# Optimization experiments

Measured on AMD Instinct MI355X. Metric: run time of the kernel, lower is better.

Reference implementation:

```python
import jax, jax.numpy as jnp
from jax import lax
import numpy as np

D = 20            # bits per code -> codebook size K = 2**D
K = 2 ** D
TEMP = 0.005
EPS = 1e-10
XSPLIT = 16
ALPHA = 1.0


def setup_inputs() -> dict:
    key = jax.random.key(0)
    x = jax.random.normal(key, (2, 128, D), dtype=jnp.float32)  # [B, N, d]
    return {"x": x}


def _book_t():
    # Deterministic {-1,+1} codebook, transposed: [D, K]
    idx = jnp.arange(K, dtype=jnp.int32)
    shifts = jnp.arange(D - 1, -1, -1, dtype=jnp.int32)
    bits = ((idx[:, None] >> shifts[None, :]) & 1).astype(jnp.float32)  # [K, D]
    return (bits * 2.0 - 1.0).T  # [D, K]


def _forward(x):
    B, N, _ = x.shape
    book_t = _book_t()                      # [D, K]
    num_splits = N // XSPLIT
    # [num_splits, B, XSPLIT, D] chunks, scanned to bound peak memory (mirrors torch chunking)
    xc = x.reshape(B, num_splits, XSPLIT, D).transpose(1, 0, 2, 3)

    def step(carry, x_chunk):
        entro_mean, mean_probs = carry
        l = (x_chunk @ book_t) / TEMP                    # [B, XSPLIT, K]
        probs = jax.nn.softmax(l, axis=-1)
        log_probs = jax.nn.log_softmax(l + EPS, axis=-1)  # eps shift, as in torch
        entropy = -jnp.sum(probs * log_probs, axis=-1)    # [B, XSPLIT]
        entro_mean = entro_mean + jnp.sum(entropy, axis=-1) / N
        # torch: probs.mean over all but last dim -> [K], broadcast-added to [B,K]
        mean_probs = mean_probs + probs.mean(axis=(0, 1))
        return (entro_mean, mean_probs), None

    init = (jnp.zeros((B,), x.dtype), jnp.zeros((K,), x.dtype))
    (entro_mean, mean_probs), _ = lax.scan(jax.checkpoint(step), init, xc)

    mean_probs = mean_probs / num_splits
    # torch mean_probs rows are identical across batch, so mean over batch == single row value
    mean_entro = -jnp.sum(mean_probs * jnp.log(mean_probs + EPS))
    entro_mean_s = entro_mean.mean()
    entro_loss = ALPHA * entro_mean_s - ALPHA * mean_entro

    q_hard = jnp.where(x > 0, 1.0, -1.0).astype(x.dtype)
    q = x + lax.stop_gradient(q_hard - x)                 # straight-through estimator
    commit_loss = jnp.mean((x - lax.stop_gradient(q)) ** 2)
    return q, entro_mean_s, mean_entro, entro_loss, commit_loss


def reference(x):
    return _forward(x)
```

## Files before the change

kernel.cpp:

```cpp
#include <hip/hip_runtime.h>
#include <math.h>


#define RS 264
#define VTS 260
#define POISON 0xAAAAAAAAu

typedef float f32x4 __attribute__((ext_vector_type(4)));
typedef short bf16x8 __attribute__((ext_vector_type(8)));

__device__ inline unsigned pk_bf16x2(float a, float b) {
  unsigned ua = __float_as_uint(a); ua += 0x7FFFu + ((ua >> 16) & 1u);
  unsigned ub = __float_as_uint(b); ub += 0x7FFFu + ((ub >> 16) & 1u);
  return (ua >> 16) | (ub & 0xFFFF0000u);
}

__global__ __launch_bounds__(256) void lfq_one(
    const float* __restrict__ x, float* __restrict__ out,
    double* __restrict__ entPart, double* __restrict__ comPart,
    double* __restrict__ mePart, unsigned* __restrict__ counter) {
  const int blk = blockIdx.x;
  const int tid = threadIdx.x;

  __shared__ float sP1[20][256];
  __shared__ float sVAH[8][VTS], sVAL[8][VTS];
  __shared__ float sVBH[8][VTS], sVBL[8][VTS];
  __shared__ unsigned short sA[64 * RS];
  __shared__ unsigned short sB[64 * RS];
  __shared__ double red[256];
  __shared__ float hb[20], cb[20];
  __shared__ int lastBlk;

  {
    const int t = tid;
    float xv[20];
    const float4* xp = (const float4*)(x + t * 20);
#pragma unroll
    for (int k = 0; k < 5; ++k) {
      float4 v = xp[k];
      xv[4 * k + 0] = v.x; xv[4 * k + 1] = v.y;
      xv[4 * k + 2] = v.z; xv[4 * k + 3] = v.w;
    }
#pragma unroll
    for (int j = 0; j < 20; ++j) {
      float z = 400.f * xv[j];
      float az = fabsf(z);
      float e = __expf(-az);
      float s = e / (1.f + e);
      sP1[j][t] = (z >= 0.f) ? (1.f - s) : s;
    }
  }
  if (tid < 20) {
    float xv = x[blk * 20 + tid];
    float z = 400.f * xv, az = fabsf(z);
    float e = __expf(-az), s = e / (1.f + e);
    hb[tid] = log1pf(e) + az * s;
    float qv = (xv > 0.f) ? 1.f : -1.f;
    out[blk * 20 + tid] = qv;
    float dx = xv - qv;
    cb[tid] = dx * dx;
  }
  __syncthreads();
  if (tid == 0) {
    float hs = 0.f, cs = 0.f;
#pragma unroll
    for (int j = 0; j < 20; ++j) { hs += hb[j]; cs += cb[j]; }
    entPart[blk] = (double)hs;
    comPart[blk] = (double)cs;
  }

  {
    const int t = tid;
    const int ahi = blk & 15, bhi = blk >> 4;
    float c = 1.f;
#pragma unroll
    for (int j = 0; j < 4; ++j) {
      float p = sP1[j][t];
      c *= ((ahi >> (3 - j)) & 1) ? p : (1.f - p);
    }
#pragma unroll
    for (int j = 0; j < 4; ++j) {
      float p = sP1[10 + j][t];
      c *= ((bhi >> (3 - j)) & 1) ? p : (1.f - p);
    }
    float p4 = sP1[4][t], p5 = sP1[5][t], p6 = sP1[6][t];
    float p7 = sP1[7][t], p8 = sP1[8][t], p9 = sP1[9][t];
    float pe = sP1[14][t], pf = sP1[15][t], pg = sP1[16][t];
    float ph = sP1[17][t], pi = sP1[18][t], pj = sP1[19][t];
#pragma unroll
    for (int g = 0; g < 8; ++g) {
      sVAH[g][t] = c * ((g & 4) ? p4 : 1.f - p4) * ((g & 2) ? p5 : 1.f - p5)
                     * ((g & 1) ? p6 : 1.f - p6);
      sVAL[g][t] =     ((g & 4) ? p7 : 1.f - p7) * ((g & 2) ? p8 : 1.f - p8)
                     * ((g & 1) ? p9 : 1.f - p9);
      sVBH[g][t] =     ((g & 4) ? pe : 1.f - pe) * ((g & 2) ? pf : 1.f - pf)
                     * ((g & 1) ? pg : 1.f - pg);
      sVBL[g][t] =     ((g & 4) ? ph : 1.f - ph) * ((g & 2) ? pi : 1.f - pi)
                     * ((g & 1) ? pj : 1.f - pj);
    }
  }
  __syncthreads();

  {
    const int r = tid & 63, tc = tid >> 6;
    const int gH = r >> 3, gL = r & 7;
    unsigned short* arow = sA + r * RS;
    unsigned short* brow = sB + r * RS;
#pragma unroll
    for (int it = 0; it < 16; ++it) {
      int t = tc * 64 + it * 4;
      float4 h = *(const float4*)&sVAH[gH][t];
      float4 l = *(const float4*)&sVAL[gL][t];
      unsigned lo = pk_bf16x2(h.x * l.x, h.y * l.y);
      unsigned hi = pk_bf16x2(h.z * l.z, h.w * l.w);
      *(uint2*)(arow + t) = make_uint2(lo, hi);
      float4 h2 = *(const float4*)&sVBH[gH][t];
      float4 l2 = *(const float4*)&sVBL[gL][t];
      unsigned lo2 = pk_bf16x2(h2.x * l2.x, h2.y * l2.y);
      unsigned hi2 = pk_bf16x2(h2.z * l2.z, h2.w * l2.w);
      *(uint2*)(brow + t) = make_uint2(lo2, hi2);
    }
  }
  __syncthreads();

  const int lane = tid & 63, w = tid >> 6;
  const int m16 = lane & 15, q = lane >> 4;
  f32x4 acc[4];
#pragma unroll
  for (int ct = 0; ct < 4; ++ct) acc[ct] = (f32x4){0.f, 0.f, 0.f, 0.f};
  const unsigned short* ap = sA + (w * 16 + m16) * RS + q * 8;
  const unsigned short* bp = sB + m16 * RS + q * 8;
#pragma unroll
  for (int ks = 0; ks < 8; ++ks) {
    bf16x8 af = *(const bf16x8*)(ap + ks * 32);
    bf16x8 b0 = *(const bf16x8*)(bp + ks * 32);
    bf16x8 b1 = *(const bf16x8*)(bp + 16 * RS + ks * 32);
    bf16x8 b2 = *(const bf16x8*)(bp + 32 * RS + ks * 32);
    bf16x8 b3 = *(const bf16x8*)(bp + 48 * RS + ks * 32);
    acc[0] = __builtin_amdgcn_mfma_f32_16x16x32_bf16(af, b0, acc[0], 0, 0, 0);
    acc[1] = __builtin_amdgcn_mfma_f32_16x16x32_bf16(af, b1, acc[1], 0, 0, 0);
    acc[2] = __builtin_amdgcn_mfma_f32_16x16x32_bf16(af, b2, acc[2], 0, 0, 0);
    acc[3] = __builtin_amdgcn_mfma_f32_16x16x32_bf16(af, b3, acc[3], 0, 0, 0);
  }

  float ts = 0.f;
#pragma unroll
  for (int ct = 0; ct < 4; ++ct)
#pragma unroll
    for (int i = 0; i < 4; ++i) {
      float m = acc[ct][i] * (1.f / 256.f);
      ts -= m * __logf(m + 1e-10f);
    }
  red[tid] = (double)ts;
  __syncthreads();
  for (int s = 128; s > 0; s >>= 1) {
    if (tid < s) red[tid] += red[tid + s];
    __syncthreads();
  }
  if (tid == 0) {
    mePart[blk] = red[0];
    __threadfence();
    unsigned old = atomicAdd(counter, 1u);
    lastBlk = ((old - POISON) == 255u) ? 1 : 0;
  }
  __syncthreads();

  if (lastBlk) {
    __threadfence();
    __shared__ double r1[256], r2[256], r3[256];
    r1[tid] = entPart[tid];
    r2[tid] = comPart[tid];
    r3[tid] = mePart[tid];
    __syncthreads();
    for (int s = 128; s > 0; s >>= 1) {
      if (tid < s) {
        r1[tid] += r1[tid + s];
        r2[tid] += r2[tid + s];
        r3[tid] += r3[tid + s];
      }
      __syncthreads();
    }
    if (tid == 0) {
      double em = r1[0] / 256.0;
      double cm = r2[0] / 5120.0;
      double me = r3[0];
      out[5120] = (float)em;
      out[5121] = (float)me;
      out[5122] = (float)(em - me);
      out[5123] = (float)cm;
    }
  }
}

extern "C" void kernel_launch(void* const* d_in, const int* in_sizes, int n_in,
                              void* d_out, int out_size, void* d_ws, size_t ws_size,
                              hipStream_t stream) {
  const float* x = (const float*)d_in[0];
  float* out = (float*)d_out;
  char* ws = (char*)d_ws;
  double* entPart = (double*)(ws);
  double* comPart = (double*)(ws + 2048);
  double* mePart  = (double*)(ws + 4096);
  unsigned* counter = (unsigned*)(ws + 6144);

  lfq_one<<<256, 256, 0, stream>>>(x, out, entPart, comPart, mePart, counter);
}
```

Measured before the change: 64.57 us.

## Double block threads and build bf16 panels directly from registers

Each block now runs 512 threads. Half of them build the A-side panel and half the B-side panel, computing the sigmoid probabilities and their products in registers and writing bf16 straight to one shared panel. This removes the intermediate sP1/sVAH/sVAL shared arrays and two barriers. The 64x64 MFMA product is split over 8 waves, each producing two 16x16 tiles, so per-wave latency drops. The costs are a deeper block reduction and scalar 2-byte shared stores that may cause bank conflicts.

```diff
diff --git a/kernel.cpp b/kernel.cpp
--- a/kernel.cpp
+++ b/kernel.cpp
@@ -3,53 +3,29 @@
 
 
 #define RS 264
-#define VTS 260
 #define POISON 0xAAAAAAAAu
 
 typedef float f32x4 __attribute__((ext_vector_type(4)));
 typedef short bf16x8 __attribute__((ext_vector_type(8)));
 
-__device__ inline unsigned pk_bf16x2(float a, float b) {
-  unsigned ua = __float_as_uint(a); ua += 0x7FFFu + ((ua >> 16) & 1u);
-  unsigned ub = __float_as_uint(b); ub += 0x7FFFu + ((ub >> 16) & 1u);
-  return (ua >> 16) | (ub & 0xFFFF0000u);
+__device__ inline unsigned short pk_bf16(float a) {
+  unsigned ua = __float_as_uint(a);
+  ua += 0x7FFFu + ((ua >> 16) & 1u);
+  return (unsigned short)(ua >> 16);
 }
 
-__global__ __launch_bounds__(256) void lfq_one(
+__global__ __launch_bounds__(512) void lfq_one(
     const float* __restrict__ x, float* __restrict__ out,
     double* __restrict__ entPart, double* __restrict__ comPart,
     double* __restrict__ mePart, unsigned* __restrict__ counter) {
   const int blk = blockIdx.x;
   const int tid = threadIdx.x;
 
-  __shared__ float sP1[20][256];
-  __shared__ float sVAH[8][VTS], sVAL[8][VTS];
-  __shared__ float sVBH[8][VTS], sVBL[8][VTS];
-  __shared__ unsigned short sA[64 * RS];
-  __shared__ unsigned short sB[64 * RS];
-  __shared__ double red[256];
+  __shared__ unsigned short sP[128 * RS];
+  __shared__ double red[512];
   __shared__ float hb[20], cb[20];
   __shared__ int lastBlk;
 
-  {
-    const int t = tid;
-    float xv[20];
-    const float4* xp = (const float4*)(x + t * 20);
-#pragma unroll
-    for (int k = 0; k < 5; ++k) {
-      float4 v = xp[k];
-      xv[4 * k + 0] = v.x; xv[4 * k + 1] = v.y;
-      xv[4 * k + 2] = v.z; xv[4 * k + 3] = v.w;
-    }
-#pragma unroll
-    for (int j = 0; j < 20; ++j) {
-      float z = 400.f * xv[j];
-      float az = fabsf(z);
-      float e = __expf(-az);
-      float s = e / (1.f + e);
-      sP1[j][t] = (z >= 0.f) ? (1.f - s) : s;
-    }
-  }
   if (tid < 20) {
     float xv = x[blk * 20 + tid];
     float z = 400.f * xv, az = fabsf(z);
@@ -60,7 +36,46 @@
     float dx = xv - qv;
     cb[tid] = dx * dx;
   }
+
+  {
+    const int side = tid >> 8;
+    const int t = tid & 255;
+    const int jo = side * 10;
+    const int hi4 = side ? (blk >> 4) : (blk & 15);
+
+    float p[10];
+    const float2* xp = (const float2*)(x + t * 20 + jo);
+#pragma unroll
+    for (int k = 0; k < 5; ++k) {
+      float2 v = xp[k];
+      float zz0 = 400.f * v.x, zz1 = 400.f * v.y;
+      float a0 = fabsf(zz0), a1 = fabsf(zz1);
+      float e0 = __expf(-a0), e1 = __expf(-a1);
+      float s0 = e0 / (1.f + e0), s1 = e1 / (1.f + e1);
+      p[2 * k]     = (zz0 >= 0.f) ? (1.f - s0) : s0;
+      p[2 * k + 1] = (zz1 >= 0.f) ? (1.f - s1) : s1;
+    }
+    float c = 1.f;
+#pragma unroll
+    for (int j = 0; j < 4; ++j)
+      c *= ((hi4 >> (3 - j)) & 1) ? p[j] : (1.f - p[j]);
+    float cvh[8], vl[8];
+#pragma unroll
+    for (int g = 0; g < 8; ++g) {
+      cvh[g] = c * ((g & 4) ? p[4] : 1.f - p[4])
+                 * ((g & 2) ? p[5] : 1.f - p[5])
+                 * ((g & 1) ? p[6] : 1.f - p[6]);
+      vl[g]  =     ((g & 4) ? p[7] : 1.f - p[7])
+                 * ((g & 2) ? p[8] : 1.f - p[8])
+                 * ((g & 1) ? p[9] : 1.f - p[9]);
+    }
+    unsigned short* panel = sP + side * 64 * RS;
+#pragma unroll
+    for (int r = 0; r < 64; ++r)
+      panel[r * RS + t] = pk_bf16(cvh[r >> 3] * vl[r & 7]);
+  }
   __syncthreads();
+
   if (tid == 0) {
     float hs = 0.f, cs = 0.f;
 #pragma unroll
@@ -69,91 +84,31 @@
     comPart[blk] = (double)cs;
   }
 
-  {
-    const int t = tid;
-    const int ahi = blk & 15, bhi = blk >> 4;
-    float c = 1.f;
-#pragma unroll
-    for (int j = 0; j < 4; ++j) {
-      float p = sP1[j][t];
-      c *= ((ahi >> (3 - j)) & 1) ? p : (1.f - p);
-    }
-#pragma unroll
-    for (int j = 0; j < 4; ++j) {
-      float p = sP1[10 + j][t];
-      c *= ((bhi >> (3 - j)) & 1) ? p : (1.f - p);
-    }
-    float p4 = sP1[4][t], p5 = sP1[5][t], p6 = sP1[6][t];
-    float p7 = sP1[7][t], p8 = sP1[8][t], p9 = sP1[9][t];
-    float pe = sP1[14][t], pf = sP1[15][t], pg = sP1[16][t];
-    float ph = sP1[17][t], pi = sP1[18][t], pj = sP1[19][t];
-#pragma unroll
-    for (int g = 0; g < 8; ++g) {
-      sVAH[g][t] = c * ((g & 4) ? p4 : 1.f - p4) * ((g & 2) ? p5 : 1.f - p5)
-                     * ((g & 1) ? p6 : 1.f - p6);
-      sVAL[g][t] =     ((g & 4) ? p7 : 1.f - p7) * ((g & 2) ? p8 : 1.f - p8)
-                     * ((g & 1) ? p9 : 1.f - p9);
-      sVBH[g][t] =     ((g & 4) ? pe : 1.f - pe) * ((g & 2) ? pf : 1.f - pf)
-                     * ((g & 1) ? pg : 1.f - pg);
-      sVBL[g][t] =     ((g & 4) ? ph : 1.f - ph) * ((g & 2) ? pi : 1.f - pi)
-                     * ((g & 1) ? pj : 1.f - pj);
-    }
-  }
-  __syncthreads();
-
-  {
-    const int r = tid & 63, tc = tid >> 6;
-    const int gH = r >> 3, gL = r & 7;
-    unsigned short* arow = sA + r * RS;
-    unsigned short* brow = sB + r * RS;
-#pragma unroll
-    for (int it = 0; it < 16; ++it) {
-      int t = tc * 64 + it * 4;
-      float4 h = *(const float4*)&sVAH[gH][t];
-      float4 l = *(const float4*)&sVAL[gL][t];
-      unsigned lo = pk_bf16x2(h.x * l.x, h.y * l.y);
-      unsigned hi = pk_bf16x2(h.z * l.z, h.w * l.w);
-      *(uint2*)(arow + t) = make_uint2(lo, hi);
-      float4 h2 = *(const float4*)&sVBH[gH][t];
-      float4 l2 = *(const float4*)&sVBL[gL][t];
-      unsigned lo2 = pk_bf16x2(h2.x * l2.x, h2.y * l2.y);
-      unsigned hi2 = pk_bf16x2(h2.z * l2.z, h2.w * l2.w);
-      *(uint2*)(brow + t) = make_uint2(lo2, hi2);
-    }
-  }
-  __syncthreads();
-
   const int lane = tid & 63, w = tid >> 6;
   const int m16 = lane & 15, q = lane >> 4;
-  f32x4 acc[4];
-#pragma unroll
-  for (int ct = 0; ct < 4; ++ct) acc[ct] = (f32x4){0.f, 0.f, 0.f, 0.f};
-  const unsigned short* ap = sA + (w * 16 + m16) * RS + q * 8;
-  const unsigned short* bp = sB + m16 * RS + q * 8;
+  const unsigned short* ap = sP + ((w & 3) * 16 + m16) * RS + q * 8;
+  const unsigned short* bp = sP + (64 + (w >> 2) * 32 + m16) * RS + q * 8;
+  f32x4 acc0 = {0.f, 0.f, 0.f, 0.f}, acc1 = {0.f, 0.f, 0.f, 0.f};
 #pragma unroll
   for (int ks = 0; ks < 8; ++ks) {
     bf16x8 af = *(const bf16x8*)(ap + ks * 32);
     bf16x8 b0 = *(const bf16x8*)(bp + ks * 32);
     bf16x8 b1 = *(const bf16x8*)(bp + 16 * RS + ks * 32);
-    bf16x8 b2 = *(const bf16x8*)(bp + 32 * RS + ks * 32);
-    bf16x8 b3 = *(const bf16x8*)(bp + 48 * RS + ks * 32);
-    acc[0] = __builtin_amdgcn_mfma_f32_16x16x32_bf16(af, b0, acc[0], 0, 0, 0);
-    acc[1] = __builtin_amdgcn_mfma_f32_16x16x32_bf16(af, b1, acc[1], 0, 0, 0);
-    acc[2] = __builtin_amdgcn_mfma_f32_16x16x32_bf16(af, b2, acc[2], 0, 0, 0);
-    acc[3] = __builtin_amdgcn_mfma_f32_16x16x32_bf16(af, b3, acc[3], 0, 0, 0);
+    acc0 = __builtin_amdgcn_mfma_f32_16x16x32_bf16(af, b0, acc0, 0, 0, 0);
+    acc1 = __builtin_amdgcn_mfma_f32_16x16x32_bf16(af, b1, acc1, 0, 0, 0);
   }
 
   float ts = 0.f;
 #pragma unroll
-  for (int ct = 0; ct < 4; ++ct)
-#pragma unroll
-    for (int i = 0; i < 4; ++i) {
-      float m = acc[ct][i] * (1.f / 256.f);
-      ts -= m * __logf(m + 1e-10f);
-    }
+  for (int i = 0; i < 4; ++i) {
+    float m0 = acc0[i] * (1.f / 256.f);
+    ts -= m0 * __logf(m0 + 1e-10f);
+    float m1 = acc1[i] * (1.f / 256.f);
+    ts -= m1 * __logf(m1 + 1e-10f);
+  }
   red[tid] = (double)ts;
   __syncthreads();
-  for (int s = 128; s > 0; s >>= 1) {
+  for (int s = 256; s > 0; s >>= 1) {
     if (tid < s) red[tid] += red[tid + s];
     __syncthreads();
   }
@@ -168,9 +123,11 @@
   if (lastBlk) {
     __threadfence();
     __shared__ double r1[256], r2[256], r3[256];
-    r1[tid] = entPart[tid];
-    r2[tid] = comPart[tid];
-    r3[tid] = mePart[tid];
+    if (tid < 256) {
+      r1[tid] = entPart[tid];
+      r2[tid] = comPart[tid];
+      r3[tid] = mePart[tid];
+    }
     __syncthreads();
     for (int s = 128; s > 0; s >>= 1) {
       if (tid < s) {
@@ -203,5 +160,5 @@
   double* mePart  = (double*)(ws + 4096);
   unsigned* counter = (unsigned*)(ws + 6144);
 
-  lfq_one<<<256, 256, 0, stream>>>(x, out, entPart, comPart, mePart, counter);
+  lfq_one<<<256, 512, 0, stream>>>(x, out, entPart, comPart, mePart, counter);
 }
```

After: 63.09 us. 2.3% less time.
